# Performance work log

Measured on AMD Instinct MI355X. Metric: run time of the kernel, lower is better.

## Reference

```python
import jax, jax.numpy as jnp
import numpy as np

N = 100000   # nodes
E = 500000   # edges
H = 128      # h_dim
TAU = 1.0    # gumbel-softmax temperature (module default)


def setup_inputs() -> dict:
    key = jax.random.key(0)
    k = jax.random.split(key, 6)
    h = jax.random.normal(k[0], (N, H), dtype=jnp.float32)
    W1 = jax.random.normal(k[1], (2 * H, H // 2), dtype=jnp.float32) / np.float32(np.sqrt(2 * H))
    b1 = jnp.zeros((H // 2,), dtype=jnp.float32)
    W2 = jax.random.normal(k[2], (H // 2, 1), dtype=jnp.float32) / np.float32(np.sqrt(H // 2))
    b2 = jnp.zeros((1,), dtype=jnp.float32)
    u = jax.random.uniform(k[3], (E, 2), dtype=jnp.float32, minval=1e-6, maxval=1.0)
    edge_index = jax.random.randint(k[4], (2, E), 0, N, dtype=jnp.int32)
    return {"h": h, "W1": W1, "b1": b1, "W2": W2, "b2": b2, "u": u, "edge_index": edge_index}


def reference(h, W1, b1, W2, b2, u, edge_index):
    row, col = edge_index[0], edge_index[1]
    # gather endpoint features and concat: [E, 2H]
    edge_feat = jnp.concatenate([h[row], h[col]], axis=-1)
    # 2-layer MLP scorer -> per-edge logit [E]
    hid = jax.nn.relu(edge_feat @ W1 + b1)
    logits = (hid @ W2 + b2)[:, 0]
    # binary gumbel-softmax over [keep-logit=0, logit]
    samp_logits = jnp.stack([jnp.zeros_like(logits), logits], axis=-1)  # [E, 2]
    g = -jnp.log(-jnp.log(u))  # gumbel noise from uniform
    y_soft = jax.nn.softmax((samp_logits + g) / TAU, axis=-1)
    # hard=True straight-through
    idx = jnp.argmax(y_soft, axis=-1)
    y_hard = jax.nn.one_hot(idx, 2, dtype=y_soft.dtype)
    y = y_hard - jax.lax.stop_gradient(y_soft) + y_soft
    weights = y[:, 1]
    return (weights, logits)
```

## Files before the change

kernel.cpp:

```cpp
#include <hip/hip_runtime.h>
#include <math.h>

#define NN 100000
#define NE 500000

typedef short bf16x8 __attribute__((ext_vector_type(8)));
typedef float f32x4  __attribute__((ext_vector_type(4)));

static __device__ __forceinline__ unsigned short f2bf_rne(float x) {
    unsigned int u = __builtin_bit_cast(unsigned int, x);
    unsigned int r = u + 0x7fffu + ((u >> 16) & 1u);
    return (unsigned short)(r >> 16);
}
static __device__ __forceinline__ float bf2f(unsigned short b) {
    return __builtin_bit_cast(float, (unsigned int)b << 16);
}

__global__ __launch_bounds__(256)
void prepack_w(const float* __restrict__ W1, unsigned short* __restrict__ WPh,
               unsigned short* __restrict__ WPl)
{
    int idx = blockIdx.x * 256 + threadIdx.x;
    int e  = idx & 7;
    int l  = (idx >> 3) & 63;
    int kt = (idx >> 9) & 3;
    int jt = idx >> 11;
    int k = kt * 32 + (l >> 4) * 8 + e;
    int j = jt * 16 + (l & 15);
    float w = (j < 64) ? W1[k * 64 + j] : W1[(128 + k) * 64 + (j - 64)];
    unsigned short hb = f2bf_rne(w);
    unsigned short lb = f2bf_rne(w - bf2f(hb));
    WPh[idx] = hb;
    WPl[idx] = lb;
}

__global__ __launch_bounds__(256)
void mfma_proj(const float* __restrict__ h, const unsigned short* __restrict__ WPh,
               const unsigned short* __restrict__ WPl, const float* __restrict__ b1,
               float* __restrict__ AB, int nnodes)
{
    const int t  = threadIdx.x;
    const int wv = t >> 6;
    const int l  = t & 63;
    const int lr = l & 15;
    const int q  = l >> 4;
    const int n0 = blockIdx.x * 64 + wv * 16;
    const int arow = n0 + lr;
    const bool aval = (arow < nnodes);

    bf16x8 ah[4];
    const float* hrow = h + (size_t)arow * 128;
#pragma unroll
    for (int kt = 0; kt < 4; ++kt) {
        float4 x0 = make_float4(0.f, 0.f, 0.f, 0.f);
        float4 x1 = make_float4(0.f, 0.f, 0.f, 0.f);
        if (aval) {
            x0 = *(const float4*)&hrow[kt * 32 + q * 8];
            x1 = *(const float4*)&hrow[kt * 32 + q * 8 + 4];
        }
        float xs[8] = {x0.x, x0.y, x0.z, x0.w, x1.x, x1.y, x1.z, x1.w};
        union { bf16x8 v; unsigned short u[8]; } H;
#pragma unroll
        for (int e = 0; e < 8; ++e)
            H.u[e] = (unsigned short)(__builtin_bit_cast(unsigned int, xs[e]) >> 16);
        ah[kt] = H.v;
    }

    const int drow = n0 + q * 4;

#pragma unroll
    for (int jt = 0; jt < 8; ++jt) {
        f32x4 acc = {0.f, 0.f, 0.f, 0.f};
#pragma unroll
        for (int kt = 0; kt < 4; ++kt) {
            const int fb = ((jt * 4 + kt) * 64 + l) * 8;
            bf16x8 bh = *(const bf16x8*)(WPh + fb);
            bf16x8 bl = *(const bf16x8*)(WPl + fb);
            acc = __builtin_amdgcn_mfma_f32_16x16x32_bf16(ah[kt], bh, acc, 0, 0, 0);
            acc = __builtin_amdgcn_mfma_f32_16x16x32_bf16(ah[kt], bl, acc, 0, 0, 0);
        }
        const int j = jt * 16 + lr;
        const float bias = (jt < 4) ? b1[j] : 0.f;
#pragma unroll
        for (int r = 0; r < 4; ++r) {
            int n = drow + r;
            if (n < nnodes) AB[(size_t)n * 128 + j] = acc[r] + bias;
        }
    }
}

__global__ __launch_bounds__(256)
void edge_sample(const float* __restrict__ AB, const float* __restrict__ h,
                 const float* __restrict__ W1, const float* __restrict__ b1,
                 const float* __restrict__ W2, const float* __restrict__ b2,
                 const float* __restrict__ u, const int* __restrict__ ei,
                 float* __restrict__ out)
{
    int t = threadIdx.x;
    int l = t & 15;
    int e = blockIdx.x * 16 + (t >> 4);

    int row = ei[e];
    int col = ei[NE + e];

    float4 a = *(const float4*)&AB[(size_t)row * 128 + l * 4];
    float4 b = *(const float4*)&AB[(size_t)col * 128 + 64 + l * 4];
    float4 w = *(const float4*)&W2[l * 4];

    float h0 = fmaxf(a.x + b.x, 0.f);
    float h1 = fmaxf(a.y + b.y, 0.f);
    float h2 = fmaxf(a.z + b.z, 0.f);
    float h3 = fmaxf(a.w + b.w, 0.f);

    float p = h0 * w.x + h1 * w.y + h2 * w.z + h3 * w.w;
    p += __shfl_xor(p, 1);
    p += __shfl_xor(p, 2);
    p += __shfl_xor(p, 4);
    p += __shfl_xor(p, 8);

    float logit = p + b2[0];
    float g0 = 0.f, g1 = 0.f, dec = 0.f;
    if (l == 0) {
        float u0 = u[2 * e];
        float u1 = u[2 * e + 1];
        g0 = -logf(-logf(u0));
        g1 = -logf(-logf(u1));
        dec = (logit + g1) - g0;
    }
    int base = (t & 63) & ~15;
    float dec_b = __shfl(dec, base);

    if (fabsf(dec_b) < 0.02f) {
        float4 bb = *(const float4*)&b1[l * 4];
        float a0 = bb.x, a1 = bb.y, a2 = bb.z, a3 = bb.w;
        const float* hr = h + (size_t)row * 128;
        const float* hc = h + (size_t)col * 128;
        for (int k4 = 0; k4 < 32; ++k4) {
            float4 hv = *(const float4*)&hr[k4 * 4];
#pragma unroll
            for (int kk = 0; kk < 4; ++kk) {
                float4 wr = *(const float4*)&W1[(k4 * 4 + kk) * 64 + l * 4];
                float hval = (&hv.x)[kk];
                a0 += hval * wr.x; a1 += hval * wr.y;
                a2 += hval * wr.z; a3 += hval * wr.w;
            }
        }
        for (int k4 = 0; k4 < 32; ++k4) {
            float4 hv = *(const float4*)&hc[k4 * 4];
#pragma unroll
            for (int kk = 0; kk < 4; ++kk) {
                float4 wr = *(const float4*)&W1[(128 + k4 * 4 + kk) * 64 + l * 4];
                float hval = (&hv.x)[kk];
                a0 += hval * wr.x; a1 += hval * wr.y;
                a2 += hval * wr.z; a3 += hval * wr.w;
            }
        }
        float r0 = fmaxf(a0, 0.f), r1 = fmaxf(a1, 0.f);
        float r2 = fmaxf(a2, 0.f), r3 = fmaxf(a3, 0.f);
        float p2 = r0 * w.x + r1 * w.y + r2 * w.z + r3 * w.w;
        p2 += __shfl_xor(p2, 1);
        p2 += __shfl_xor(p2, 2);
        p2 += __shfl_xor(p2, 4);
        p2 += __shfl_xor(p2, 8);
        logit = p2 + b2[0];
    }

    if (l == 0) {
        out[e]      = (logit + g1 > g0) ? 1.0f : 0.0f;
        out[NE + e] = logit;
    }
}

__global__ __launch_bounds__(256)
void node_proj(const float* __restrict__ h, const float* __restrict__ W1,
               const float* __restrict__ b1, float* __restrict__ AB, int nnodes)
{
    __shared__ float lh[64 * 132];

    const int t   = threadIdx.x;
    const int tj  = t & 15;
    const int tnf = t >> 4;
    const int n0  = blockIdx.x * 64;

#pragma unroll
    for (int i = 0; i < 8; ++i) {
        int flat = i * 256 + t;
        int nl = flat >> 5;
        int c  = flat & 31;
        int ng = n0 + nl;
        float4 v = make_float4(0.f, 0.f, 0.f, 0.f);
        if (ng < nnodes) v = *(const float4*)&h[(size_t)ng * 128 + c * 4];
        *(float4*)&lh[nl * 132 + c * 4] = v;
    }
    __syncthreads();

    const float* wa_base = W1 + tj * 4;
    const float* wb_base = W1 + 128 * 64 + tj * 4;

    float acc[4][8];
    {
        float4 bv = *(const float4*)&b1[tj * 4];
#pragma unroll
        for (int r = 0; r < 4; ++r) {
            acc[r][0] = bv.x; acc[r][1] = bv.y; acc[r][2] = bv.z; acc[r][3] = bv.w;
            acc[r][4] = 0.f;  acc[r][5] = 0.f;  acc[r][6] = 0.f;  acc[r][7] = 0.f;
        }
    }

    float4 A0[4], B0[4], A1[4], B1[4];
#pragma unroll
    for (int kk = 0; kk < 4; ++kk) {
        A0[kk] = *(const float4*)&wa_base[kk * 64];
        B0[kk] = *(const float4*)&wb_base[kk * 64];
    }

#define LOAD_W(AX, BX, K4)                                              \
    _Pragma("unroll")                                                   \
    for (int kk = 0; kk < 4; ++kk) {                                    \
        AX[kk] = *(const float4*)&wa_base[((K4) * 4 + kk) * 64];        \
        BX[kk] = *(const float4*)&wb_base[((K4) * 4 + kk) * 64];        \
    }

#define COMPUTE(AX, BX, K4)                                             \
    {                                                                   \
        float4 hv[4];                                                   \
        _Pragma("unroll")                                               \
        for (int r = 0; r < 4; ++r)                                     \
            hv[r] = *(const float4*)&lh[(tnf + 16 * r) * 132 + (K4) * 4]; \
        _Pragma("unroll")                                               \
        for (int kk = 0; kk < 4; ++kk) {                                \
            float4 wa = AX[kk], wb = BX[kk];                            \
            _Pragma("unroll")                                           \
            for (int r = 0; r < 4; ++r) {                               \
                float hk = (kk == 0) ? hv[r].x : (kk == 1) ? hv[r].y    \
                         : (kk == 2) ? hv[r].z : hv[r].w;               \
                acc[r][0] += hk * wa.x;                                 \
                acc[r][1] += hk * wa.y;                                 \
                acc[r][2] += hk * wa.z;                                 \
                acc[r][3] += hk * wa.w;                                 \
                acc[r][4] += hk * wb.x;                                 \
                acc[r][5] += hk * wb.y;                                 \
                acc[r][6] += hk * wb.z;                                 \
                acc[r][7] += hk * wb.w;                                 \
            }                                                           \
        }                                                               \
    }

#pragma unroll 1
    for (int k4 = 0; k4 < 30; k4 += 2) {
        LOAD_W(A1, B1, k4 + 1)
        COMPUTE(A0, B0, k4)
        LOAD_W(A0, B0, k4 + 2)
        COMPUTE(A1, B1, k4 + 1)
    }
    LOAD_W(A1, B1, 31)
    COMPUTE(A0, B0, 30)
    COMPUTE(A1, B1, 31)

#undef LOAD_W
#undef COMPUTE

#pragma unroll
    for (int r = 0; r < 4; ++r) {
        int ng = n0 + tnf + 16 * r;
        if (ng >= nnodes) continue;
        float* orow = AB + (size_t)ng * 128;
        *(float4*)&orow[tj * 4]      = make_float4(acc[r][0], acc[r][1], acc[r][2], acc[r][3]);
        *(float4*)&orow[64 + tj * 4] = make_float4(acc[r][4], acc[r][5], acc[r][6], acc[r][7]);
    }
}

__global__ __launch_bounds__(256)
void edge_direct(const float* __restrict__ h, const float* __restrict__ W1,
                 const float* __restrict__ b1, const float* __restrict__ W2,
                 const float* __restrict__ b2, const float* __restrict__ u,
                 const int* __restrict__ ei, float* __restrict__ out)
{
    int t = threadIdx.x;
    int l = t & 15;
    int e = blockIdx.x * 16 + (t >> 4);

    int row = ei[e];
    int col = ei[NE + e];

    float a0 = 0.f, a1 = 0.f, a2 = 0.f, a3 = 0.f;
    const float* hr = h + (size_t)row * 128;
    const float* hc = h + (size_t)col * 128;

    for (int k4 = 0; k4 < 32; ++k4) {
        float4 hv = *(const float4*)&hr[k4 * 4];
#pragma unroll
        for (int kk = 0; kk < 4; ++kk) {
            float4 wr = *(const float4*)&W1[(k4 * 4 + kk) * 64 + l * 4];
            float hval = (&hv.x)[kk];
            a0 += hval * wr.x; a1 += hval * wr.y; a2 += hval * wr.z; a3 += hval * wr.w;
        }
    }
    for (int k4 = 0; k4 < 32; ++k4) {
        float4 hv = *(const float4*)&hc[k4 * 4];
#pragma unroll
        for (int kk = 0; kk < 4; ++kk) {
            float4 wr = *(const float4*)&W1[(128 + k4 * 4 + kk) * 64 + l * 4];
            float hval = (&hv.x)[kk];
            a0 += hval * wr.x; a1 += hval * wr.y; a2 += hval * wr.z; a3 += hval * wr.w;
        }
    }
    float4 bb = *(const float4*)&b1[l * 4];
    float4 w  = *(const float4*)&W2[l * 4];
    float h0 = fmaxf(a0 + bb.x, 0.f);
    float h1 = fmaxf(a1 + bb.y, 0.f);
    float h2 = fmaxf(a2 + bb.z, 0.f);
    float h3 = fmaxf(a3 + bb.w, 0.f);

    float p = h0 * w.x + h1 * w.y + h2 * w.z + h3 * w.w;
    p += __shfl_xor(p, 1);
    p += __shfl_xor(p, 2);
    p += __shfl_xor(p, 4);
    p += __shfl_xor(p, 8);

    if (l == 0) {
        float logit = p + b2[0];
        float u0 = u[2 * e];
        float u1 = u[2 * e + 1];
        float g0 = -logf(-logf(u0));
        float g1 = -logf(-logf(u1));
        out[e]      = (logit + g1 > g0) ? 1.0f : 0.0f;
        out[NE + e] = logit;
    }
}

extern "C" void kernel_launch(void* const* d_in, const int* in_sizes, int n_in,
                              void* d_out, int out_size, void* d_ws, size_t ws_size,
                              hipStream_t stream)
{
    const float* h  = (const float*)d_in[0];
    const float* W1 = (const float*)d_in[1];
    const float* b1 = (const float*)d_in[2];
    const float* W2 = (const float*)d_in[3];
    const float* b2 = (const float*)d_in[4];
    const float* u  = (const float*)d_in[5];
    const int*   ei = (const int*)d_in[6];
    float* out = (float*)d_out;

    const size_t ab_bytes = (size_t)NN * 128 * sizeof(float);
    const size_t wp_bytes = 2u * 16384u * sizeof(unsigned short);
    float* AB = (float*)d_ws;

    if (ws_size >= ab_bytes + wp_bytes) {
        unsigned short* WPh = (unsigned short*)((char*)d_ws + ab_bytes);
        unsigned short* WPl = WPh + 16384;
        prepack_w<<<64, 256, 0, stream>>>(W1, WPh, WPl);
        mfma_proj<<<(NN + 63) / 64, 256, 0, stream>>>(h, WPh, WPl, b1, AB, NN);
        edge_sample<<<NE / 16, 256, 0, stream>>>(AB, h, W1, b1, W2, b2, u, ei, out);
    } else if (ws_size >= ab_bytes) {
        node_proj<<<(NN + 63) / 64, 256, 0, stream>>>(h, W1, b1, AB, NN);
        edge_sample<<<NE / 16, 256, 0, stream>>>(AB, h, W1, b1, W2, b2, u, ei, out);
    } else {
        edge_direct<<<NE / 16, 256, 0, stream>>>(h, W1, b1, W2, b2, u, ei, out);
    }
}
```

Before: 115.8 us.

## Defer near-boundary exact recompute to a compacted worklist kernel

The edge sampling kernel no longer runs the exact fp32 MLP recompute inline for edges whose decision lies close to the threshold. Instead it records those edge ids in a global list through an atomic counter. A separate small grid-stride kernel then recomputes only the listed edges and overwrites their outputs. This is meant to remove divergent heavy work from the main bandwidth-bound kernel and to shrink its register and code footprint. In exchange it adds a memset, an extra launch and atomics, and it widens the margin, which sends more edges to the fix pass. The fallback path that uses node_proj also loses its recompute step.

```diff
diff --git a/kernel.cpp b/kernel.cpp
--- a/kernel.cpp
+++ b/kernel.cpp
@@ -3,6 +3,7 @@
 
 #define NN 100000
 #define NE 500000
+#define MARGIN 0.05f
 
 typedef short bf16x8 __attribute__((ext_vector_type(8)));
 typedef float f32x4  __attribute__((ext_vector_type(4)));
@@ -89,12 +90,12 @@
     }
 }
 
-__global__ __launch_bounds__(256)
-void edge_sample(const float* __restrict__ AB, const float* __restrict__ h,
-                 const float* __restrict__ W1, const float* __restrict__ b1,
-                 const float* __restrict__ W2, const float* __restrict__ b2,
-                 const float* __restrict__ u, const int* __restrict__ ei,
-                 float* __restrict__ out)
+template <bool FLAG>
+__global__ __launch_bounds__(256)
+void edge_sample(const float* __restrict__ AB, const float* __restrict__ W2,
+                 const float* __restrict__ b2, const float* __restrict__ u,
+                 const int* __restrict__ ei, float* __restrict__ out,
+                 unsigned* __restrict__ counter, int* __restrict__ list, int cap)
 {
     int t = threadIdx.x;
     int l = t & 15;
@@ -118,23 +119,48 @@
     p += __shfl_xor(p, 4);
     p += __shfl_xor(p, 8);
 
-    float logit = p + b2[0];
-    float g0 = 0.f, g1 = 0.f, dec = 0.f;
     if (l == 0) {
+        float logit = p + b2[0];
         float u0 = u[2 * e];
         float u1 = u[2 * e + 1];
-        g0 = -logf(-logf(u0));
-        g1 = -logf(-logf(u1));
-        dec = (logit + g1) - g0;
-    }
-    int base = (t & 63) & ~15;
-    float dec_b = __shfl(dec, base);
-
-    if (fabsf(dec_b) < 0.02f) {
+        float g0 = -logf(-logf(u0));
+        float g1 = -logf(-logf(u1));
+        out[e]      = (logit + g1 > g0) ? 1.0f : 0.0f;
+        out[NE + e] = logit;
+        if (FLAG) {
+            float dec = (logit + g1) - g0;
+            if (fabsf(dec) < MARGIN) {
+                unsigned idx = atomicAdd(counter, 1u);
+                if ((int)idx < cap) list[idx] = e;
+            }
+        }
+    }
+}
+
+__global__ __launch_bounds__(256)
+void edge_fix(const float* __restrict__ h, const float* __restrict__ W1,
+              const float* __restrict__ b1, const float* __restrict__ W2,
+              const float* __restrict__ b2, const float* __restrict__ u,
+              const int* __restrict__ ei, const unsigned* __restrict__ counter,
+              const int* __restrict__ list, int cap, float* __restrict__ out)
+{
+    int t = threadIdx.x;
+    int l = t & 15;
+    int gid = blockIdx.x * 16 + (t >> 4);
+    int ngroups = gridDim.x * 16;
+    unsigned cnt = *counter;
+    if ((int)cnt > cap) cnt = (unsigned)cap;
+
+    for (unsigned i = gid; i < cnt; i += ngroups) {
+        int e = list[i];
+        int row = ei[e];
+        int col = ei[NE + e];
+
         float4 bb = *(const float4*)&b1[l * 4];
         float a0 = bb.x, a1 = bb.y, a2 = bb.z, a3 = bb.w;
         const float* hr = h + (size_t)row * 128;
         const float* hc = h + (size_t)col * 128;
+
         for (int k4 = 0; k4 < 32; ++k4) {
             float4 hv = *(const float4*)&hr[k4 * 4];
 #pragma unroll
@@ -155,19 +181,24 @@
                 a2 += hval * wr.z; a3 += hval * wr.w;
             }
         }
+        float4 w = *(const float4*)&W2[l * 4];
         float r0 = fmaxf(a0, 0.f), r1 = fmaxf(a1, 0.f);
         float r2 = fmaxf(a2, 0.f), r3 = fmaxf(a3, 0.f);
-        float p2 = r0 * w.x + r1 * w.y + r2 * w.z + r3 * w.w;
-        p2 += __shfl_xor(p2, 1);
-        p2 += __shfl_xor(p2, 2);
-        p2 += __shfl_xor(p2, 4);
-        p2 += __shfl_xor(p2, 8);
-        logit = p2 + b2[0];
-    }
-
-    if (l == 0) {
-        out[e]      = (logit + g1 > g0) ? 1.0f : 0.0f;
-        out[NE + e] = logit;
+        float p = r0 * w.x + r1 * w.y + r2 * w.z + r3 * w.w;
+        p += __shfl_xor(p, 1);
+        p += __shfl_xor(p, 2);
+        p += __shfl_xor(p, 4);
+        p += __shfl_xor(p, 8);
+
+        if (l == 0) {
+            float logit = p + b2[0];
+            float u0 = u[2 * e];
+            float u1 = u[2 * e + 1];
+            float g0 = -logf(-logf(u0));
+            float g1 = -logf(-logf(u1));
+            out[e]      = (logit + g1 > g0) ? 1.0f : 0.0f;
+            out[NE + e] = logit;
+        }
     }
 }
 
@@ -344,17 +375,31 @@
 
     const size_t ab_bytes = (size_t)NN * 128 * sizeof(float);
     const size_t wp_bytes = 2u * 16384u * sizeof(unsigned short);
+    const size_t ctr_off  = ab_bytes + wp_bytes;
+    const size_t list_off = ctr_off + 256;
     float* AB = (float*)d_ws;
 
-    if (ws_size >= ab_bytes + wp_bytes) {
+    long long rem = (long long)ws_size - (long long)list_off;
+    int cap = (rem > 0) ? (int)(rem / 4) : 0;
+    if (cap > 262144) cap = 262144;
+
+    if (cap >= 16384) {
         unsigned short* WPh = (unsigned short*)((char*)d_ws + ab_bytes);
         unsigned short* WPl = WPh + 16384;
+        unsigned* counter = (unsigned*)((char*)d_ws + ctr_off);
+        int* list = (int*)((char*)d_ws + list_off);
+
+        hipMemsetAsync(counter, 0, sizeof(unsigned), stream);
         prepack_w<<<64, 256, 0, stream>>>(W1, WPh, WPl);
         mfma_proj<<<(NN + 63) / 64, 256, 0, stream>>>(h, WPh, WPl, b1, AB, NN);
-        edge_sample<<<NE / 16, 256, 0, stream>>>(AB, h, W1, b1, W2, b2, u, ei, out);
+        edge_sample<true><<<NE / 16, 256, 0, stream>>>(AB, W2, b2, u, ei, out,
+                                                       counter, list, cap);
+        edge_fix<<<128, 256, 0, stream>>>(h, W1, b1, W2, b2, u, ei,
+                                          counter, list, cap, out);
     } else if (ws_size >= ab_bytes) {
         node_proj<<<(NN + 63) / 64, 256, 0, stream>>>(h, W1, b1, AB, NN);
-        edge_sample<<<NE / 16, 256, 0, stream>>>(AB, h, W1, b1, W2, b2, u, ei, out);
+        edge_sample<false><<<NE / 16, 256, 0, stream>>>(AB, W2, b2, u, ei, out,
+                                                        nullptr, nullptr, 0);
     } else {
         edge_direct<<<NE / 16, 256, 0, stream>>>(h, W1, b1, W2, b2, u, ei, out);
     }
```

Result: slower. 243.1 us (+110.0%).
